# Optimization experiments

Hardware: AMD Instinct MI355X
Metric: run time of the kernel (lower is better)

Reference implementation:

```python
import jax, jax.numpy as jnp
import numpy as np

B, S, H, OUT, L = 32, 4096, 128, 128, 3


def _log_g(x):
    return jnp.where(x >= 0, jnp.log(jax.nn.relu(x) + 0.5), -jax.nn.softplus(-x))


def _cell(x, Wz, bz, Wh, bh):
    # x: [B, S, Din] -> h: [B, S, H]
    k = x @ Wz.T + bz                              # [B,S,H]
    log_z = -jax.nn.softplus(-k)
    log_coeffs = -jax.nn.softplus(k)
    # h_0 = zeros -> log_g(0) = log(0.5)
    log_h0 = jnp.full((x.shape[0], 1, k.shape[-1]), np.log(0.5), dtype=k.dtype)
    log_tilde_h = _log_g(x @ Wh.T + bh)
    log_values = jnp.concatenate([log_h0, log_z + log_tilde_h], axis=1)  # [B,S+1,H]
    # FAITHFUL to source: cumsum over the FEATURE axis (dim=-1), pad along seq
    a_star = jnp.pad(jnp.cumsum(log_coeffs, axis=-1), ((0, 0), (1, 0), (0, 0)))
    log_h = a_star + jax.lax.cumlogsumexp(log_values - a_star, axis=1)
    # torch forward applies sigmoid to the cell output, then drops the h_0 row
    return jax.nn.sigmoid(jnp.exp(log_h))[:, 1:, :]


def setup_inputs() -> dict:
    key = jax.random.key(0)
    ks = jax.random.split(key, 2 * L + 2)
    inp = {"x": jax.random.normal(ks[0], (B, S), dtype=jnp.float32)}
    for l in range(L):
        din = 1 if l == 0 else H
        inp[f"Wz{l}"] = jax.random.normal(ks[1 + 2 * l], (H, din), dtype=jnp.float32) * 0.02
        inp[f"bz{l}"] = jnp.zeros((H,), dtype=jnp.float32)
        inp[f"Wh{l}"] = jax.random.normal(ks[2 + 2 * l], (H, din), dtype=jnp.float32) * 0.02
        inp[f"bh{l}"] = jnp.zeros((H,), dtype=jnp.float32)
    inp["Wout"] = jax.random.normal(ks[-1], (OUT, H * S), dtype=jnp.float32) * (1.0 / np.sqrt(H * S))
    inp["bout"] = jnp.zeros((OUT,), dtype=jnp.float32)
    return inp


def reference(x, Wz0, bz0, Wh0, bh0, Wz1, bz1, Wh1, bh1, Wz2, bz2, Wh2, bh2, Wout, bout):
    h = x[:, :, None]  # [B,S,1]
    for (Wz, bz, Wh, bh) in ((Wz0, bz0, Wh0, bh0), (Wz1, bz1, Wh1, bh1), (Wz2, bz2, Wh2, bh2)):
        h = _cell(h, Wz, bz, Wh, bh)
    flat = h.reshape(h.shape[0], -1)  # [B, S*H]
    return flat @ Wout.T + bout       # [B, OUT]
```

## Files before the change

kernel.cpp:

```cpp
#include <hip/hip_runtime.h>
#include <hip/hip_bf16.h>
#include <math.h>

#define B_   32
#define S_   4096
#define H_   128
#define OUT_ 128
#define P_   (B_*S_)
#define NC_  64
#define CH_  (S_/NC_)
#define NKS_ 512
#define KTOT_ (H_*S_)
#define NEGINF_ (-__builtin_inff())
#define HTP_ 136
#define LOGHALF_ (-0.6931471805599453f)

typedef __bf16 bf16x8 __attribute__((ext_vector_type(8)));
typedef float  f32x4  __attribute__((ext_vector_type(4)));
typedef unsigned short ushort8_t __attribute__((ext_vector_type(8)));

__device__ __forceinline__ float sp_(float x) {
  return __logf(1.f + __expf(x));
}
__device__ __forceinline__ float logg_(float x) {
  float t = (x >= 0.f) ? (x + 0.5f) : __builtin_amdgcn_rcpf(1.f + __expf(-x));
  return __logf(t);
}
__device__ __forceinline__ float lae_(float a, float b) {
  float m = fmaxf(a, b);
  float d = -fabsf(a - b);
  return m + __logf(1.f + __expf(d));
}
__device__ __forceinline__ float sigm_(float e) {
  return __builtin_amdgcn_rcpf(1.f + __expf(-e));
}
__device__ __forceinline__ unsigned short f2bf_(float f) {
  unsigned int u = __float_as_uint(f);
  u += 0x7fffu + ((u >> 16) & 1u);
  return (unsigned short)(u >> 16);
}

#define DPPADD_(v, ctrl, rmask) \
  ((v) + __int_as_float(__builtin_amdgcn_update_dpp( \
      0, __float_as_int(v), (ctrl), (rmask), 0xf, true)))
__device__ __forceinline__ float wscan_(float v) {
  v = DPPADD_(v, 0x111, 0xf);
  v = DPPADD_(v, 0x112, 0xf);
  v = DPPADD_(v, 0x114, 0xf);
  v = DPPADD_(v, 0x118, 0xf);
  v = DPPADD_(v, 0x142, 0xa);
  v = DPPADD_(v, 0x143, 0xc);
  return v;
}

__global__ __launch_bounds__(256) void prep0c_kernel(
    const float* __restrict__ x,
    const float* __restrict__ Wz, const float* __restrict__ bz,
    const float* __restrict__ Wh, const float* __restrict__ bh,
    float* __restrict__ u, float* __restrict__ A, float* __restrict__ tot,
    const float* __restrict__ Wz1, const float* __restrict__ Wh1,
    const float* __restrict__ Wz2, const float* __restrict__ Wh2,
    unsigned short* __restrict__ Wc1, unsigned short* __restrict__ Wc2)
{
  __shared__ float tpart[4][128];
  if (blockIdx.x >= 2048) {
    int idx = (blockIdx.x - 2048) * 256 + threadIdx.x;
    Wc1[idx] = f2bf_(idx < 16384 ? Wz1[idx] : Wh1[idx - 16384]);
    Wc2[idx] = f2bf_(idx < 16384 ? Wz2[idx] : Wh2[idx - 16384]);
    return;
  }
  int lane = threadIdx.x & 63, w = threadIdx.x >> 6;
  float wz0 = Wz[lane], wz1 = Wz[lane + 64];
  float bz0 = bz[lane], bz1 = bz[lane + 64];
  float wh0 = Wh[lane], wh1 = Wh[lane + 64];
  float bh0 = bh[lane], bh1 = bh[lane + 64];
  int blk = blockIdx.x;
  size_t base = (size_t)blk * (CH_ * H_);
  int pos0 = blk * CH_;
  float t0 = NEGINF_, t1 = NEGINF_;
  for (int j = 0; j < 16; ++j) {
    int i = j * 4 + w;
    float xv = x[pos0 + i];
    float k0 = fmaf(xv, wz0, bz0), k1 = fmaf(xv, wz1, bz1);
    float g0 = fmaf(xv, wh0, bh0), g1 = fmaf(xv, wh1, bh1);
    float lc0 = -sp_(k0), lc1 = -sp_(k1);
    float lv0 = k0 + lc0 + logg_(g0);
    float lv1 = k1 + lc1 + logg_(g1);
    float s0 = wscan_(lc0);
    float c0 = __shfl(s0, 63, 64);
    float s1 = wscan_(lc1) + c0;
    float u0 = lv0 - s0, u1 = lv1 - s1;
    size_t o = base + (size_t)i * H_;
    u[o + lane]      = u0;  u[o + 64 + lane] = u1;
    A[o + lane]      = s0;  A[o + 64 + lane] = s1;
    t0 = lae_(t0, u0); t1 = lae_(t1, u1);
  }
  tpart[w][lane] = t0; tpart[w][64 + lane] = t1;
  __syncthreads();
  if (w == 0) {
    int ch = lane;
    tot[(size_t)blk * H_ + ch] =
        lae_(lae_(tpart[0][ch], tpart[1][ch]), lae_(tpart[2][ch], tpart[3][ch]));
    ch = lane + 64;
    tot[(size_t)blk * H_ + ch] =
        lae_(lae_(tpart[0][ch], tpart[1][ch]), lae_(tpart[2][ch], tpart[3][ch]));
  }
}

__global__ __launch_bounds__(256) void kb_kernel(
    const float* __restrict__ totIn,
    const unsigned short* __restrict__ Wc,
    const float* __restrict__ bz, const float* __restrict__ bh,
    float* __restrict__ u, float* __restrict__ A,
    float* __restrict__ totOut)
{
  __shared__ unsigned short hT[64][HTP_];
  __shared__ union {
    float kg[16][260];
    float scr[32][128];
  } ks;
  __shared__ float thand[128];
  __shared__ float tpart[4][128];
  int tid = threadIdx.x;
  int lane = tid & 63, w = tid >> 6;
  int l15 = lane & 15, quad = lane >> 4;
  int half = tid >> 7, ch = tid & 127;
  int blk = blockIdx.x;
  int cidx = blk & (NC_ - 1);
  size_t base = (size_t)blk * (CH_ * H_);

  {
    const float* tp = totIn + (size_t)(blk - cidx) * H_ + ch;
    float p0 = NEGINF_, p1 = NEGINF_;
    int i = half;
    for (; i + 2 < cidx; i += 4) {
      float a0 = tp[(size_t)i * H_];
      float a1 = tp[(size_t)(i + 2) * H_];
      p0 = lae_(p0, a0); p1 = lae_(p1, a1);
    }
    for (; i < cidx; i += 2) p0 = lae_(p0, tp[(size_t)i * H_]);
    tpart[half * 2][ch] = p0; tpart[half * 2 + 1][ch] = p1;
  }
  __syncthreads();

  if (half == 0) {
    float r = LOGHALF_;
    r = lae_(r, tpart[0][ch]); r = lae_(r, tpart[1][ch]);
    r = lae_(r, tpart[2][ch]); r = lae_(r, tpart[3][ch]);
    const float* up = u + base + ch;
    const float* Ap = A + base + ch;
    for (int i0 = 0; i0 < 32; i0 += 16) {
      float uv[16], av[16];
      #pragma unroll
      for (int i = 0; i < 16; ++i) { uv[i] = up[(i0 + i) * H_]; av[i] = Ap[(i0 + i) * H_]; }
      #pragma unroll
      for (int i = 0; i < 16; ++i) {
        r = lae_(r, uv[i]);
        hT[i0 + i][ch] = f2bf_(sigm_(__expf(av[i] + r)));
      }
    }
    thand[ch] = r;
  } else {
    float r = NEGINF_;
    const float* up = u + base + ch;
    for (int i0 = 0; i0 < 32; i0 += 16) {
      float uv[16];
      #pragma unroll
      for (int i = 0; i < 16; ++i) uv[i] = up[(32 + i0 + i) * H_];
      #pragma unroll
      for (int i = 0; i < 16; ++i) { r = lae_(r, uv[i]); ks.scr[i0 + i][ch] = r; }
    }
  }
  __syncthreads();
  if (half == 1) {
    float r31 = thand[ch];
    const float* Ap = A + base + ch;
    for (int i0 = 0; i0 < 32; i0 += 16) {
      float av[16];
      #pragma unroll
      for (int i = 0; i < 16; ++i) av[i] = Ap[(32 + i0 + i) * H_];
      #pragma unroll
      for (int i = 0; i < 16; ++i) {
        float ri = lae_(r31, ks.scr[i0 + i][ch]);
        hT[32 + i0 + i][ch] = f2bf_(sigm_(__expf(av[i] + ri)));
      }
    }
  }
  __syncthreads();

  float bz0v = bz[lane], bz1v = bz[lane + 64];
  float bh0v = bh[lane], bh1v = bh[lane + 64];
  float t0 = NEGINF_, t1 = NEGINF_;

  for (int t = 0; t < 4; ++t) {
    f32x4 z = {0.f, 0.f, 0.f, 0.f};
    f32x4 acc[4] = {z, z, z, z};
    #pragma unroll
    for (int kk = 0; kk < 4; ++kk) {
      bf16x8 a = *reinterpret_cast<const bf16x8*>(&hT[t * 16 + l15][kk * 32 + quad * 8]);
      #pragma unroll
      for (int nt = 0; nt < 4; ++nt) {
        int n = w * 64 + nt * 16 + l15;
        bf16x8 bf = *reinterpret_cast<const bf16x8*>(Wc + n * 128 + kk * 32 + quad * 8);
        acc[nt] = __builtin_amdgcn_mfma_f32_16x16x32_bf16(a, bf, acc[nt], 0, 0, 0);
      }
    }
    __syncthreads();
    #pragma unroll
    for (int nt = 0; nt < 4; ++nt) {
      int col = w * 64 + nt * 16 + l15;
      #pragma unroll
      for (int r2 = 0; r2 < 4; ++r2)
        ks.kg[quad * 4 + r2][col] = acc[nt][r2];
    }
    __syncthreads();
    #pragma unroll
    for (int i = 0; i < 4; ++i) {
      int row = w + i * 4;
      int sIdx = t * 16 + row;
      float k0 = ks.kg[row][lane]        + bz0v;
      float k1 = ks.kg[row][64 + lane]   + bz1v;
      float g0 = ks.kg[row][128 + lane]  + bh0v;
      float g1 = ks.kg[row][192 + lane]  + bh1v;
      float lc0 = -sp_(k0), lc1 = -sp_(k1);
      float lv0 = k0 + lc0 + logg_(g0);
      float lv1 = k1 + lc1 + logg_(g1);
      float s0 = wscan_(lc0);
      float c0 = __shfl(s0, 63, 64);
      float s1 = wscan_(lc1) + c0;
      float u0 = lv0 - s0, u1 = lv1 - s1;
      size_t o = base + (size_t)sIdx * H_;
      u[o + lane]      = u0;  u[o + 64 + lane] = u1;
      A[o + lane]      = s0;  A[o + 64 + lane] = s1;
      t0 = lae_(t0, u0); t1 = lae_(t1, u1);
    }
  }

  tpart[w][lane] = t0; tpart[w][64 + lane] = t1;
  __syncthreads();
  if (w == 0) {
    int c = lane;
    totOut[(size_t)blk * H_ + c] =
        lae_(lae_(tpart[0][c], tpart[1][c]), lae_(tpart[2][c], tpart[3][c]));
    c = lane + 64;
    totOut[(size_t)blk * H_ + c] =
        lae_(lae_(tpart[0][c], tpart[1][c]), lae_(tpart[2][c], tpart[3][c]));
  }
}

__global__ __launch_bounds__(256) void scan3v2_kernel(
    const float* __restrict__ u, const float* __restrict__ A,
    const float* __restrict__ totIn, unsigned short* __restrict__ hbf)
{
  __shared__ float scr[32][128];
  __shared__ float thand[128];
  __shared__ float tpart[4][128];
  int tid = threadIdx.x;
  int half = tid >> 7, ch = tid & 127;
  int blk = blockIdx.x;
  int cidx = blk & (NC_ - 1);
  size_t base = (size_t)blk * (CH_ * H_);
  const float* up = u + base + ch;
  const float* Ap = A + base + ch;
  unsigned short* hp = hbf + base + ch;

  {
    const float* tp = totIn + (size_t)(blk - cidx) * H_ + ch;
    float p0 = NEGINF_, p1 = NEGINF_;
    int i = half;
    for (; i + 2 < cidx; i += 4) {
      float a0 = tp[(size_t)i * H_];
      float a1 = tp[(size_t)(i + 2) * H_];
      p0 = lae_(p0, a0); p1 = lae_(p1, a1);
    }
    for (; i < cidx; i += 2) p0 = lae_(p0, tp[(size_t)i * H_]);
    tpart[half * 2][ch] = p0; tpart[half * 2 + 1][ch] = p1;
  }
  __syncthreads();

  if (half == 0) {
    float r = LOGHALF_;
    r = lae_(r, tpart[0][ch]); r = lae_(r, tpart[1][ch]);
    r = lae_(r, tpart[2][ch]); r = lae_(r, tpart[3][ch]);
    for (int i0 = 0; i0 < 32; i0 += 16) {
      float uv[16], av[16];
      #pragma unroll
      for (int i = 0; i < 16; ++i) { uv[i] = up[(i0 + i) * H_]; av[i] = Ap[(i0 + i) * H_]; }
      #pragma unroll
      for (int i = 0; i < 16; ++i) {
        r = lae_(r, uv[i]);
        hp[(size_t)(i0 + i) * H_] = f2bf_(sigm_(__expf(av[i] + r)));
      }
    }
    thand[ch] = r;
  } else {
    float r = NEGINF_;
    for (int i0 = 0; i0 < 32; i0 += 16) {
      float uv[16];
      #pragma unroll
      for (int i = 0; i < 16; ++i) uv[i] = up[(32 + i0 + i) * H_];
      #pragma unroll
      for (int i = 0; i < 16; ++i) { r = lae_(r, uv[i]); scr[i0 + i][ch] = r; }
    }
  }
  __syncthreads();
  if (half == 1) {
    float r31 = thand[ch];
    for (int i0 = 0; i0 < 32; i0 += 16) {
      float av[16];
      #pragma unroll
      for (int i = 0; i < 16; ++i) av[i] = Ap[(32 + i0 + i) * H_];
      #pragma unroll
      for (int i = 0; i < 16; ++i) {
        float ri = lae_(r31, scr[i0 + i][ch]);
        hp[(size_t)(32 + i0 + i) * H_] = f2bf_(sigm_(__expf(av[i] + ri)));
      }
    }
  }
}

__global__ __launch_bounds__(256) void outmm_kernel(
    const unsigned short* __restrict__ hbf,
    const float* __restrict__ Wout,
    float* __restrict__ part)
{
  const int KSL = KTOT_ / NKS_;
  int tid = threadIdx.x, w = tid >> 6, lane = tid & 63;
  int l15 = lane & 15, quad = lane >> 4;
  int k0base = blockIdx.x * KSL;
  f32x4 acc[2][2] = {{{0,0,0,0},{0,0,0,0}},{{0,0,0,0},{0,0,0,0}}};
  for (int ks = 0; ks < KSL; ks += 32) {
    int k0 = k0base + ks;
    bf16x8 a0 = *reinterpret_cast<const bf16x8*>(
        hbf + (size_t)l15 * KTOT_ + k0 + quad * 8);
    bf16x8 a1 = *reinterpret_cast<const bf16x8*>(
        hbf + (size_t)(16 + l15) * KTOT_ + k0 + quad * 8);
    #pragma unroll
    for (int nt = 0; nt < 2; ++nt) {
      int n = w * 32 + nt * 16 + l15;
      const float* wp = Wout + (size_t)n * KTOT_ + k0 + quad * 8;
      float4 wa = *reinterpret_cast<const float4*>(wp);
      float4 wb = *reinterpret_cast<const float4*>(wp + 4);
      ushort8_t tt;
      tt[0] = f2bf_(wa.x); tt[1] = f2bf_(wa.y); tt[2] = f2bf_(wa.z); tt[3] = f2bf_(wa.w);
      tt[4] = f2bf_(wb.x); tt[5] = f2bf_(wb.y); tt[6] = f2bf_(wb.z); tt[7] = f2bf_(wb.w);
      bf16x8 bf = __builtin_bit_cast(bf16x8, tt);
      acc[0][nt] = __builtin_amdgcn_mfma_f32_16x16x32_bf16(a0, bf, acc[0][nt], 0, 0, 0);
      acc[1][nt] = __builtin_amdgcn_mfma_f32_16x16x32_bf16(a1, bf, acc[1][nt], 0, 0, 0);
    }
  }
  float* pp = part + (size_t)blockIdx.x * (B_ * OUT_);
  #pragma unroll
  for (int mt = 0; mt < 2; ++mt)
    #pragma unroll
    for (int nt = 0; nt < 2; ++nt)
      #pragma unroll
      for (int r = 0; r < 4; ++r) {
        int b = mt * 16 + quad * 4 + r;
        int o = w * 32 + nt * 16 + l15;
        pp[b * OUT_ + o] = acc[mt][nt][r];
      }
}

__global__ __launch_bounds__(256) void outred_kernel(
    const float* __restrict__ part, const float* __restrict__ bout,
    float* __restrict__ out)
{
  int w = threadIdx.x >> 6, lane = threadIdx.x & 63;
  int idx = blockIdx.x * 4 + w;
  float s = 0.f;
  for (int wg = lane; wg < NKS_; wg += 64) s += part[(size_t)wg * (B_ * OUT_) + idx];
  #pragma unroll
  for (int d = 32; d; d >>= 1) s += __shfl_down(s, (unsigned)d, 64);
  if (lane == 0) out[idx] = s + bout[idx & (OUT_ - 1)];
}

extern "C" void kernel_launch(void* const* d_in, const int* in_sizes, int n_in,
                              void* d_out, int out_size, void* d_ws, size_t ws_size,
                              hipStream_t stream)
{
  const float* x    = (const float*)d_in[0];
  const float* Wz[3] = {(const float*)d_in[1], (const float*)d_in[5], (const float*)d_in[9]};
  const float* bz[3] = {(const float*)d_in[2], (const float*)d_in[6], (const float*)d_in[10]};
  const float* Wh[3] = {(const float*)d_in[3], (const float*)d_in[7], (const float*)d_in[11]};
  const float* bh[3] = {(const float*)d_in[4], (const float*)d_in[8], (const float*)d_in[12]};
  const float* Wout = (const float*)d_in[13];
  const float* bout = (const float*)d_in[14];
  float* out = (float*)d_out;

  char* ws = (char*)d_ws;
  float*          u     = (float*)(ws + 0);
  float*          A     = (float*)(ws + 67108864);
  unsigned short* hbf   = (unsigned short*)(ws + 134217728);
  unsigned short* Wc1   = (unsigned short*)(ws + 167772160);
  unsigned short* Wc2   = (unsigned short*)(ws + 167837696);
  float*          totA  = (float*)(ws + 167903232);
  float*          totB  = (float*)(ws + 168951808);
  float*          part  = (float*)(ws + 170000384);

  prep0c_kernel<<<B_ * NC_ + 128, 256, 0, stream>>>(
      x, Wz[0], bz[0], Wh[0], bh[0], u, A, totA,
      Wz[1], Wh[1], Wz[2], Wh[2], Wc1, Wc2);

  kb_kernel<<<B_ * NC_, 256, 0, stream>>>(totA, Wc1, bz[1], bh[1], u, A, totB);
  kb_kernel<<<B_ * NC_, 256, 0, stream>>>(totB, Wc2, bz[2], bh[2], u, A, totA);

  scan3v2_kernel<<<B_ * NC_, 256, 0, stream>>>(u, A, totA, hbf);

  outmm_kernel<<<NKS_, 256, 0, stream>>>(hbf, Wout, part);
  outred_kernel<<<(B_ * OUT_) / 4, 256, 0, stream>>>(part, bout, out);
}
```

Measured before the change: 658.6 us.

## Store chunk-local inclusive logsumexp prefixes so consumers apply carry-in in parallel

```diff
diff --git a/kernel.cpp b/kernel.cpp
--- a/kernel.cpp
+++ b/kernel.cpp
@@ -9,7 +9,7 @@
 #define P_   (B_*S_)
 #define NC_  64
 #define CH_  (S_/NC_)
-#define NKS_ 512
+#define NKS_ 1024
 #define KTOT_ (H_*S_)
 #define NEGINF_ (-__builtin_inff())
 #define HTP_ 136
@@ -57,12 +57,12 @@
     const float* __restrict__ x,
     const float* __restrict__ Wz, const float* __restrict__ bz,
     const float* __restrict__ Wh, const float* __restrict__ bh,
-    float* __restrict__ u, float* __restrict__ A, float* __restrict__ tot,
+    float* __restrict__ Lb, float* __restrict__ A, float* __restrict__ tot,
     const float* __restrict__ Wz1, const float* __restrict__ Wh1,
     const float* __restrict__ Wz2, const float* __restrict__ Wh2,
     unsigned short* __restrict__ Wc1, unsigned short* __restrict__ Wc2)
 {
-  __shared__ float tpart[4][128];
+  __shared__ float segw[4][128];
   if (blockIdx.x >= 2048) {
     int idx = (blockIdx.x - 2048) * 256 + threadIdx.x;
     Wc1[idx] = f2bf_(idx < 16384 ? Wz1[idx] : Wh1[idx - 16384]);
@@ -76,13 +76,16 @@
   float bh0 = bh[lane], bh1 = bh[lane + 64];
   int blk = blockIdx.x;
   size_t base = (size_t)blk * (CH_ * H_);
-  int pos0 = blk * CH_;
-  float t0 = NEGINF_, t1 = NEGINF_;
+  int pos0 = blk * CH_ + w * 16;
+  float xv[16];
+  #pragma unroll
+  for (int j = 0; j < 16; ++j) xv[j] = x[pos0 + j];
+  float L0[16], L1[16];
+  float r0 = NEGINF_, r1 = NEGINF_;
+  #pragma unroll
   for (int j = 0; j < 16; ++j) {
-    int i = j * 4 + w;
-    float xv = x[pos0 + i];
-    float k0 = fmaf(xv, wz0, bz0), k1 = fmaf(xv, wz1, bz1);
-    float g0 = fmaf(xv, wh0, bh0), g1 = fmaf(xv, wh1, bh1);
+    float k0 = fmaf(xv[j], wz0, bz0), k1 = fmaf(xv[j], wz1, bz1);
+    float g0 = fmaf(xv[j], wh0, bh0), g1 = fmaf(xv[j], wh1, bh1);
     float lc0 = -sp_(k0), lc1 = -sp_(k1);
     float lv0 = k0 + lc0 + logg_(g0);
     float lv1 = k1 + lc1 + logg_(g1);
@@ -90,20 +93,31 @@
     float c0 = __shfl(s0, 63, 64);
     float s1 = wscan_(lc1) + c0;
     float u0 = lv0 - s0, u1 = lv1 - s1;
-    size_t o = base + (size_t)i * H_;
-    u[o + lane]      = u0;  u[o + 64 + lane] = u1;
-    A[o + lane]      = s0;  A[o + 64 + lane] = s1;
-    t0 = lae_(t0, u0); t1 = lae_(t1, u1);
-  }
-  tpart[w][lane] = t0; tpart[w][64 + lane] = t1;
+    r0 = lae_(r0, u0); r1 = lae_(r1, u1);
+    L0[j] = r0; L1[j] = r1;
+    size_t o = base + (size_t)(w * 16 + j) * H_;
+    A[o + lane] = s0; A[o + 64 + lane] = s1;
+  }
+  segw[w][lane] = r0; segw[w][lane + 64] = r1;
   __syncthreads();
+  float p0 = NEGINF_, p1 = NEGINF_;
+  for (int jj = 0; jj < w; ++jj) {
+    p0 = lae_(p0, segw[jj][lane]);
+    p1 = lae_(p1, segw[jj][lane + 64]);
+  }
+  #pragma unroll
+  for (int j = 0; j < 16; ++j) {
+    size_t o = base + (size_t)(w * 16 + j) * H_;
+    Lb[o + lane]      = lae_(p0, L0[j]);
+    Lb[o + 64 + lane] = lae_(p1, L1[j]);
+  }
   if (w == 0) {
-    int ch = lane;
-    tot[(size_t)blk * H_ + ch] =
-        lae_(lae_(tpart[0][ch], tpart[1][ch]), lae_(tpart[2][ch], tpart[3][ch]));
-    ch = lane + 64;
-    tot[(size_t)blk * H_ + ch] =
-        lae_(lae_(tpart[0][ch], tpart[1][ch]), lae_(tpart[2][ch], tpart[3][ch]));
+    float q0 = lae_(lae_(segw[0][lane], segw[1][lane]),
+                    lae_(segw[2][lane], segw[3][lane]));
+    float q1 = lae_(lae_(segw[0][lane + 64], segw[1][lane + 64]),
+                    lae_(segw[2][lane + 64], segw[3][lane + 64]));
+    tot[(size_t)blk * H_ + lane] = q0;
+    tot[(size_t)blk * H_ + 64 + lane] = q1;
   }
 }
 
@@ -111,16 +125,12 @@
     const float* __restrict__ totIn,
     const unsigned short* __restrict__ Wc,
     const float* __restrict__ bz, const float* __restrict__ bh,
-    float* __restrict__ u, float* __restrict__ A,
+    float* __restrict__ Lb, float* __restrict__ A,
     float* __restrict__ totOut)
 {
   __shared__ unsigned short hT[64][HTP_];
-  __shared__ union {
-    float kg[16][260];
-    float scr[32][128];
-  } ks;
-  __shared__ float thand[128];
-  __shared__ float tpart[4][128];
+  __shared__ float kg[16][260];
+  __shared__ float segw[4][128];
   int tid = threadIdx.x;
   int lane = tid & 63, w = tid >> 6;
   int l15 = lane & 15, quad = lane >> 4;
@@ -139,50 +149,23 @@
       p0 = lae_(p0, a0); p1 = lae_(p1, a1);
     }
     for (; i < cidx; i += 2) p0 = lae_(p0, tp[(size_t)i * H_]);
-    tpart[half * 2][ch] = p0; tpart[half * 2 + 1][ch] = p1;
+    segw[half * 2][ch] = p0; segw[half * 2 + 1][ch] = p1;
   }
   __syncthreads();
 
-  if (half == 0) {
+  {
     float r = LOGHALF_;
-    r = lae_(r, tpart[0][ch]); r = lae_(r, tpart[1][ch]);
-    r = lae_(r, tpart[2][ch]); r = lae_(r, tpart[3][ch]);
-    const float* up = u + base + ch;
-    const float* Ap = A + base + ch;
+    r = lae_(r, segw[0][ch]); r = lae_(r, segw[1][ch]);
+    r = lae_(r, segw[2][ch]); r = lae_(r, segw[3][ch]);
+    const float* Lp = Lb + base + (size_t)half * 32 * H_ + ch;
+    const float* Ap = A  + base + (size_t)half * 32 * H_ + ch;
     for (int i0 = 0; i0 < 32; i0 += 16) {
-      float uv[16], av[16];
-      #pragma unroll
-      for (int i = 0; i < 16; ++i) { uv[i] = up[(i0 + i) * H_]; av[i] = Ap[(i0 + i) * H_]; }
+      float Lv[16], Av[16];
+      #pragma unroll
+      for (int i = 0; i < 16; ++i) { Lv[i] = Lp[(i0 + i) * H_]; Av[i] = Ap[(i0 + i) * H_]; }
       #pragma unroll
       for (int i = 0; i < 16; ++i) {
-        r = lae_(r, uv[i]);
-        hT[i0 + i][ch] = f2bf_(sigm_(__expf(av[i] + r)));
-      }
-    }
-    thand[ch] = r;
-  } else {
-    float r = NEGINF_;
-    const float* up = u + base + ch;
-    for (int i0 = 0; i0 < 32; i0 += 16) {
-      float uv[16];
-      #pragma unroll
-      for (int i = 0; i < 16; ++i) uv[i] = up[(32 + i0 + i) * H_];
-      #pragma unroll
-      for (int i = 0; i < 16; ++i) { r = lae_(r, uv[i]); ks.scr[i0 + i][ch] = r; }
-    }
-  }
-  __syncthreads();
-  if (half == 1) {
-    float r31 = thand[ch];
-    const float* Ap = A + base + ch;
-    for (int i0 = 0; i0 < 32; i0 += 16) {
-      float av[16];
-      #pragma unroll
-      for (int i = 0; i < 16; ++i) av[i] = Ap[(32 + i0 + i) * H_];
-      #pragma unroll
-      for (int i = 0; i < 16; ++i) {
-        float ri = lae_(r31, ks.scr[i0 + i][ch]);
-        hT[32 + i0 + i][ch] = f2bf_(sigm_(__expf(av[i] + ri)));
+        hT[half * 32 + i0 + i][ch] = f2bf_(sigm_(__expf(Av[i] + lae_(r, Lv[i]))));
       }
     }
   }
@@ -190,7 +173,7 @@
 
   float bz0v = bz[lane], bz1v = bz[lane + 64];
   float bh0v = bh[lane], bh1v = bh[lane + 64];
-  float t0 = NEGINF_, t1 = NEGINF_;
+  float R0 = NEGINF_, R1 = NEGINF_;
 
   for (int t = 0; t < 4; ++t) {
     f32x4 z = {0.f, 0.f, 0.f, 0.f};
@@ -211,17 +194,19 @@
       int col = w * 64 + nt * 16 + l15;
       #pragma unroll
       for (int r2 = 0; r2 < 4; ++r2)
-        ks.kg[quad * 4 + r2][col] = acc[nt][r2];
+        kg[quad * 4 + r2][col] = acc[nt][r2];
     }
     __syncthreads();
+    float ll0[4], ll1[4];
+    float lr0 = NEGINF_, lr1 = NEGINF_;
     #pragma unroll
     for (int i = 0; i < 4; ++i) {
-      int row = w + i * 4;
+      int row = w * 4 + i;
       int sIdx = t * 16 + row;
-      float k0 = ks.kg[row][lane]        + bz0v;
-      float k1 = ks.kg[row][64 + lane]   + bz1v;
-      float g0 = ks.kg[row][128 + lane]  + bh0v;
-      float g1 = ks.kg[row][192 + lane]  + bh1v;
+      float k0 = kg[row][lane]        + bz0v;
+      float k1 = kg[row][64 + lane]   + bz1v;
+      float g0 = kg[row][128 + lane]  + bh0v;
+      float g1 = kg[row][192 + lane]  + bh1v;
       float lc0 = -sp_(k0), lc1 = -sp_(k1);
       float lv0 = k0 + lc0 + logg_(g0);
       float lv1 = k1 + lc1 + logg_(g1);
@@ -229,40 +214,46 @@
       float c0 = __shfl(s0, 63, 64);
       float s1 = wscan_(lc1) + c0;
       float u0 = lv0 - s0, u1 = lv1 - s1;
+      lr0 = lae_(lr0, u0); lr1 = lae_(lr1, u1);
+      ll0[i] = lr0; ll1[i] = lr1;
       size_t o = base + (size_t)sIdx * H_;
-      u[o + lane]      = u0;  u[o + 64 + lane] = u1;
-      A[o + lane]      = s0;  A[o + 64 + lane] = s1;
-      t0 = lae_(t0, u0); t1 = lae_(t1, u1);
-    }
-  }
-
-  tpart[w][lane] = t0; tpart[w][64 + lane] = t1;
-  __syncthreads();
+      A[o + lane] = s0;  A[o + 64 + lane] = s1;
+    }
+    segw[w][lane] = lr0; segw[w][lane + 64] = lr1;
+    __syncthreads();
+    float p0 = R0, p1 = R1;
+    for (int jj = 0; jj < w; ++jj) {
+      p0 = lae_(p0, segw[jj][lane]);
+      p1 = lae_(p1, segw[jj][lane + 64]);
+    }
+    #pragma unroll
+    for (int i = 0; i < 4; ++i) {
+      size_t o = base + (size_t)(t * 16 + w * 4 + i) * H_;
+      Lb[o + lane]      = lae_(p0, ll0[i]);
+      Lb[o + 64 + lane] = lae_(p1, ll1[i]);
+    }
+    R0 = lae_(R0, lae_(lae_(segw[0][lane], segw[1][lane]),
+                       lae_(segw[2][lane], segw[3][lane])));
+    R1 = lae_(R1, lae_(lae_(segw[0][lane + 64], segw[1][lane + 64]),
+                       lae_(segw[2][lane + 64], segw[3][lane + 64])));
+  }
+
   if (w == 0) {
-    int c = lane;
-    totOut[(size_t)blk * H_ + c] =
-        lae_(lae_(tpart[0][c], tpart[1][c]), lae_(tpart[2][c], tpart[3][c]));
-    c = lane + 64;
-    totOut[(size_t)blk * H_ + c] =
-        lae_(lae_(tpart[0][c], tpart[1][c]), lae_(tpart[2][c], tpart[3][c]));
+    totOut[(size_t)blk * H_ + lane] = R0;
+    totOut[(size_t)blk * H_ + 64 + lane] = R1;
   }
 }
 
 __global__ __launch_bounds__(256) void scan3v2_kernel(
-    const float* __restrict__ u, const float* __restrict__ A,
+    const float* __restrict__ Lb, const float* __restrict__ A,
     const float* __restrict__ totIn, unsigned short* __restrict__ hbf)
 {
-  __shared__ float scr[32][128];
-  __shared__ float thand[128];
   __shared__ float tpart[4][128];
   int tid = threadIdx.x;
   int half = tid >> 7, ch = tid & 127;
   int blk = blockIdx.x;
   int cidx = blk & (NC_ - 1);
   size_t base = (size_t)blk * (CH_ * H_);
-  const float* up = u + base + ch;
-  const float* Ap = A + base + ch;
-  unsigned short* hp = hbf + base + ch;
 
   {
     const float* tp = totIn + (size_t)(blk - cidx) * H_ + ch;
@@ -278,43 +269,19 @@
   }
   __syncthreads();
 
-  if (half == 0) {
-    float r = LOGHALF_;
-    r = lae_(r, tpart[0][ch]); r = lae_(r, tpart[1][ch]);
-    r = lae_(r, tpart[2][ch]); r = lae_(r, tpart[3][ch]);
-    for (int i0 = 0; i0 < 32; i0 += 16) {
-      float uv[16], av[16];
-      #pragma unroll
-      for (int i = 0; i < 16; ++i) { uv[i] = up[(i0 + i) * H_]; av[i] = Ap[(i0 + i) * H_]; }
-      #pragma unroll
-      for (int i = 0; i < 16; ++i) {
-        r = lae_(r, uv[i]);
-        hp[(size_t)(i0 + i) * H_] = f2bf_(sigm_(__expf(av[i] + r)));
-      }
-    }
-    thand[ch] = r;
-  } else {
-    float r = NEGINF_;
-    for (int i0 = 0; i0 < 32; i0 += 16) {
-      float uv[16];
-      #pragma unroll
-      for (int i = 0; i < 16; ++i) uv[i] = up[(32 + i0 + i) * H_];
-      #pragma unroll
-      for (int i = 0; i < 16; ++i) { r = lae_(r, uv[i]); scr[i0 + i][ch] = r; }
-    }
-  }
-  __syncthreads();
-  if (half == 1) {
-    float r31 = thand[ch];
-    for (int i0 = 0; i0 < 32; i0 += 16) {
-      float av[16];
-      #pragma unroll
-      for (int i = 0; i < 16; ++i) av[i] = Ap[(32 + i0 + i) * H_];
-      #pragma unroll
-      for (int i = 0; i < 16; ++i) {
-        float ri = lae_(r31, scr[i0 + i][ch]);
-        hp[(size_t)(32 + i0 + i) * H_] = f2bf_(sigm_(__expf(av[i] + ri)));
-      }
+  float r = LOGHALF_;
+  r = lae_(r, tpart[0][ch]); r = lae_(r, tpart[1][ch]);
+  r = lae_(r, tpart[2][ch]); r = lae_(r, tpart[3][ch]);
+  const float* Lp = Lb + base + (size_t)half * 32 * H_ + ch;
+  const float* Ap = A  + base + (size_t)half * 32 * H_ + ch;
+  unsigned short* hp = hbf + base + (size_t)half * 32 * H_ + ch;
+  for (int i0 = 0; i0 < 32; i0 += 16) {
+    float Lv[16], Av[16];
+    #pragma unroll
+    for (int i = 0; i < 16; ++i) { Lv[i] = Lp[(i0 + i) * H_]; Av[i] = Ap[(i0 + i) * H_]; }
+    #pragma unroll
+    for (int i = 0; i < 16; ++i) {
+      hp[(size_t)(i0 + i) * H_] = f2bf_(sigm_(__expf(Av[i] + lae_(r, Lv[i]))));
     }
   }
 }
@@ -389,23 +356,23 @@
   float* out = (float*)d_out;
 
   char* ws = (char*)d_ws;
-  float*          u     = (float*)(ws + 0);
+  float*          Lb    = (float*)(ws + 0);
   float*          A     = (float*)(ws + 67108864);
   unsigned short* hbf   = (unsigned short*)(ws + 134217728);
   unsigned short* Wc1   = (unsigned short*)(ws + 167772160);
   unsigned short* Wc2   = (unsigned short*)(ws + 167837696);
   float*          totA  = (float*)(ws + 167903232);
   float*          totB  = (float*)(ws + 168951808);
-  float*          part  = (float*)(ws + 170000384);
+  float*          part  = (float*)(ws + 0);
 
   prep0c_kernel<<<B_ * NC_ + 128, 256, 0, stream>>>(
-      x, Wz[0], bz[0], Wh[0], bh[0], u, A, totA,
+      x, Wz[0], bz[0], Wh[0], bh[0], Lb, A, totA,
       Wz[1], Wh[1], Wz[2], Wh[2], Wc1, Wc2);
 
-  kb_kernel<<<B_ * NC_, 256, 0, stream>>>(totA, Wc1, bz[1], bh[1], u, A, totB);
-  kb_kernel<<<B_ * NC_, 256, 0, stream>>>(totB, Wc2, bz[2], bh[2], u, A, totA);
-
-  scan3v2_kernel<<<B_ * NC_, 256, 0, stream>>>(u, A, totA, hbf);
+  kb_kernel<<<B_ * NC_, 256, 0, stream>>>(totA, Wc1, bz[1], bh[1], Lb, A, totB);
+  kb_kernel<<<B_ * NC_, 256, 0, stream>>>(totB, Wc2, bz[2], bh[2], Lb, A, totA);
+
+  scan3v2_kernel<<<B_ * NC_, 256, 0, stream>>>(Lb, A, totA, hbf);
 
   outmm_kernel<<<NKS_, 256, 0, stream>>>(hbf, Wout, part);
   outred_kernel<<<(B_ * OUT_) / 4, 256, 0, stream>>>(part, bout, out);
```

New measurement: 681.5 us. +3.5%, slower.
